# Kernel tuning notes

Measured on AMD Instinct MI355X. Metric: run time of the kernel, lower is better.

The kernel has to match this reference:

```python
import jax, jax.numpy as jnp
import numpy as np

N_NODES = 100000
N_EDGES = 1600000
D_IN, D_HID, D_OUT = 256, 128, 64


def setup_inputs() -> dict:
    key = jax.random.key(0)
    k = jax.random.split(key, 6)
    x = jax.random.normal(k[0], (N_NODES, D_IN), dtype=jnp.float32)
    edge_index = jax.random.randint(k[1], (2, N_EDGES), 0, N_NODES, dtype=jnp.int64)
    W1 = jax.random.normal(k[2], (D_IN, D_HID), dtype=jnp.float32) / np.sqrt(D_IN)
    b1 = jnp.zeros((D_HID,), dtype=jnp.float32)
    W2 = jax.random.normal(k[3], (D_HID, D_OUT), dtype=jnp.float32) / np.sqrt(D_HID)
    b2 = jnp.zeros((D_OUT,), dtype=jnp.float32)
    return {"x": x, "edge_index": edge_index, "W1": W1, "b1": b1, "W2": W2, "b2": b2}


def gcn_conv(x, W, b, src, dst, n):
    """PyG GCNConv: h = D^-1/2 (A+I) D^-1/2 (x W) + b, symmetric norm with self-loops."""
    h = x @ W                                           # [n, d_out]
    # degree from destination (col) index, +1 for the self-loop edge weight
    deg = jnp.ones((n,), x.dtype).at[dst].add(jnp.float32(1.0))
    dinv = jax.lax.rsqrt(deg)                           # deg >= 1, no inf
    norm = dinv[src] * dinv[dst]                        # [E]
    agg = jax.ops.segment_sum(h[src] * norm[:, None], dst, num_segments=n)
    agg = agg + h * (dinv * dinv)[:, None]              # self-loop contribution
    return agg + b


def reference(x, edge_index, W1, b1, W2, b2):
    src, dst = edge_index[0], edge_index[1]
    n = x.shape[0]
    h = gcn_conv(x, W1, b1, src, dst, n)
    h = jax.nn.relu(h)                                  # dropout is identity in eval mode
    out = gcn_conv(h, W2, b2, src, dst, n)
    return out
```

## Files before the change

### kernel.cpp

```cpp
#include <hip/hip_runtime.h>
#include <stdint.h>

typedef unsigned short u16;
typedef unsigned int u32;
typedef __bf16 bf16x8 __attribute__((ext_vector_type(8)));
typedef float floatx4 __attribute__((ext_vector_type(4)));

static __device__ __forceinline__ float bf2f(u16 u) {
  union { u32 i; float f; } v; v.i = ((u32)u) << 16; return v.f;
}
static __device__ __forceinline__ u16 f2bf(float f) {
  union { float f; u32 i; } v; v.f = f;
  u32 u = v.i;
  return (u16)((u + 0x7fffu + ((u >> 16) & 1u)) >> 16);
}

__global__ void k_edgemode(const int* __restrict__ ei, int* __restrict__ flag) {
  int t = threadIdx.x;
  int v = ei[2 * t + 1];
  unsigned long long b = __ballot(v == 0);
  if (t == 0) *flag = (b == ~0ull) ? 1 : 0;
}

static __device__ __forceinline__ int edge_src(const int* ei, int E, int i, int m64) {
  return m64 ? ei[2 * (size_t)i] : ei[i];
}
static __device__ __forceinline__ int edge_dst(const int* ei, int E, int i, int m64) {
  return m64 ? ei[2 * (size_t)E + 2 * (size_t)i] : ei[(size_t)E + i];
}

__global__ void k_transpose(const float* __restrict__ W1, const float* __restrict__ W2,
                            u16* __restrict__ Wt1, u16* __restrict__ Wt2) {
  int i = blockIdx.x * 256 + threadIdx.x;
  if (i < 256 * 128) {
    int k = i >> 7, c = i & 127;
    Wt1[c * 256 + k] = f2bf(W1[i]);
  } else {
    int j = i - 256 * 128;
    if (j < 128 * 64) {
      int k = j >> 6, c = j & 63;
      Wt2[c * 128 + k] = f2bf(W2[j]);
    }
  }
}

#define CHUNK 2048

__global__ void k_count(const int* __restrict__ ei, int E, const int* __restrict__ flag,
                        int* __restrict__ bucket_cnt, int NB) {
  __shared__ int h[1024];
  const int t = threadIdx.x;
  for (int i = t; i < 1024; i += 256) h[i] = 0;
  __syncthreads();
  const int c0 = blockIdx.x * CHUNK;
  const int cnt = min(CHUNK, E - c0);
  const int m64 = *flag;
  for (int i = t; i < cnt; i += 256)
    atomicAdd(&h[edge_dst(ei, E, c0 + i, m64) >> 7], 1);
  __syncthreads();
  for (int i = t; i < NB; i += 256)
    if (h[i]) atomicAdd(&bucket_cnt[i], h[i]);
}

__global__ void k_bscan(const int* __restrict__ bucket_cnt, int* __restrict__ bucket_base,
                        int* __restrict__ bucket_cursor, int NB,
                        int* __restrict__ row_ptr, int n, int E) {
  __shared__ int ts[256];
  const int t = threadIdx.x;
  const int b4 = t * 4;
  int a0 = (b4 + 0 < NB) ? bucket_cnt[b4 + 0] : 0;
  int a1 = (b4 + 1 < NB) ? bucket_cnt[b4 + 1] : 0;
  int a2 = (b4 + 2 < NB) ? bucket_cnt[b4 + 2] : 0;
  int a3 = (b4 + 3 < NB) ? bucket_cnt[b4 + 3] : 0;
  int p1 = a0, p2 = p1 + a1, p3 = p2 + a2, tsum = p3 + a3;
  ts[t] = tsum;
  __syncthreads();
  for (int off = 1; off < 256; off <<= 1) {
    int x = (t >= off) ? ts[t - off] : 0;
    __syncthreads();
    ts[t] += x;
    __syncthreads();
  }
  int ex0 = ts[t] - tsum;
  int e[4] = {ex0, ex0 + p1, ex0 + p2, ex0 + p3};
#pragma unroll
  for (int j = 0; j < 4; ++j) {
    int i = b4 + j;
    if (i < NB) { bucket_base[i] = e[j]; bucket_cursor[i] = e[j]; }
  }
  if (t == 0) row_ptr[n] = E + n;
}

__global__ void k_place(const int* __restrict__ ei, int E, const int* __restrict__ flag,
                        int* __restrict__ bucket_cursor, uint2* __restrict__ pairs, int NB) {
  __shared__ int h[1024];
  __shared__ int ex[1024];
  __shared__ int cur[1024];
  __shared__ int ts[256];
  __shared__ uint2 stage[CHUNK];
  const int t = threadIdx.x;
  const int c0 = blockIdx.x * CHUNK;
  const int cnt = min(CHUNK, E - c0);
  const int m64 = *flag;

  for (int i = t; i < 1024; i += 256) h[i] = 0;
  __syncthreads();

  int es[8], ed[8];
#pragma unroll
  for (int j = 0; j < 8; ++j) {
    int i = t + j * 256;
    es[j] = 0; ed[j] = -1;
    if (i < cnt) {
      es[j] = edge_src(ei, E, c0 + i, m64);
      ed[j] = edge_dst(ei, E, c0 + i, m64);
      atomicAdd(&h[ed[j] >> 7], 1);
    }
  }
  __syncthreads();

  const int b4 = t * 4;
  int a0 = h[b4], a1 = h[b4 + 1], a2 = h[b4 + 2], a3 = h[b4 + 3];
  int p1 = a0, p2 = p1 + a1, p3 = p2 + a2, tsum = p3 + a3;
  ts[t] = tsum;
  __syncthreads();
  for (int off = 1; off < 256; off <<= 1) {
    int x = (t >= off) ? ts[t - off] : 0;
    __syncthreads();
    ts[t] += x;
    __syncthreads();
  }
  int ex0 = ts[t] - tsum;
  ex[b4] = ex0;       cur[b4] = ex0;
  ex[b4 + 1] = ex0 + p1; cur[b4 + 1] = ex0 + p1;
  ex[b4 + 2] = ex0 + p2; cur[b4 + 2] = ex0 + p2;
  ex[b4 + 3] = ex0 + p3; cur[b4 + 3] = ex0 + p3;
  __syncthreads();

#pragma unroll
  for (int j = 0; j < 8; ++j) {
    if (ed[j] >= 0) {
      int b = ed[j] >> 7;
      int pos = atomicAdd(&cur[b], 1);
      stage[pos] = make_uint2((u32)es[j], (u32)ed[j]);
    }
  }
  __syncthreads();
  for (int i = t; i < NB; i += 256) {
    int c = h[i];
    if (c > 0) h[i] = atomicAdd(&bucket_cursor[i], c);
  }
  __syncthreads();

  for (int i = t; i < cnt; i += 256) {
    uint2 p = stage[i];
    int b = (int)(p.y >> 7);
    pairs[h[b] + (i - ex[b])] = p;
  }
}

#define BMAX 3072
__global__ void k_csr(const uint2* __restrict__ pairs, const int* __restrict__ bucket_cnt,
                      const int* __restrict__ bucket_base, int* __restrict__ row_ptr,
                      float* __restrict__ dinv, int* __restrict__ srcs, int n) {
  __shared__ int h[128], cur[128];
  __shared__ int lsrc[BMAX];
  const int b = blockIdx.x;
  const int t = threadIdx.x;
  const int cnt = bucket_cnt[b];
  const int base = bucket_base[b];
  const int nbase = base + b * 128;

  if (t < 128) h[t] = 0;
  __syncthreads();
  for (int i = t; i < cnt; i += 256)
    atomicAdd(&h[pairs[base + i].y & 127], 1);
  __syncthreads();

  __shared__ int sc[128];
  int v = 0;
  if (t < 128) { v = h[t]; sc[t] = v; }
  __syncthreads();
  for (int off = 1; off < 128; off <<= 1) {
    int x = 0;
    if (t < 128 && t >= off) x = sc[t - off];
    __syncthreads();
    if (t < 128) sc[t] += x;
    __syncthreads();
  }
  if (t < 128) {
    int excl = sc[t] - v;
    cur[t] = excl + t + 1;
    int node = b * 128 + t;
    if (node < n) {
      row_ptr[node] = nbase + excl + t;
      dinv[node] = rsqrtf(1.0f + (float)v);
      int sp = excl + t;
      if (sp < BMAX) lsrc[sp] = node;
      else srcs[nbase + sp] = node;
    }
  }
  __syncthreads();

  for (int i = t; i < cnt; i += 256) {
    uint2 p = pairs[base + i];
    int pos = atomicAdd(&cur[p.y & 127], 1);
    if (pos < BMAX) lsrc[pos] = (int)p.x;
    else srcs[nbase + pos] = (int)p.x;
  }
  __syncthreads();
  const int lim = min(cnt + 128, BMAX);
  for (int i = t; i < lim; i += 256) srcs[nbase + i] = lsrc[i];
}

template<int N, int K, bool A_FP32>
__launch_bounds__(256, 4)
__global__ void k_gemm(const void* __restrict__ Ap, const u16* __restrict__ Wt,
                       const float* __restrict__ dinv, u16* __restrict__ G, int M)
{
  constexpr int ESZ = A_FP32 ? 4 : 2;
  constexpr int KS  = K / 32;
  constexpr int NT  = N / 32;
  const int t = threadIdx.x;
  const int wave = t >> 6, lane = t & 63;
  const int row0 = blockIdx.x * 64;
  const int wr = wave >> 1, wc = wave & 1;
  const int lm = lane & 15, lq = lane >> 4;

  floatx4 acc[2][NT];
#pragma unroll
  for (int i = 0; i < 2; ++i)
#pragma unroll
    for (int j = 0; j < NT; ++j) acc[i][j] = (floatx4)(0.0f);

  int r0 = row0 + wr * 32 + lm;
  int r1 = r0 + 16;
  if (r0 >= M) r0 = M - 1;
  if (r1 >= M) r1 = M - 1;
  const char* pa0 = (const char*)Ap + ((size_t)r0 * K + lq * 8) * ESZ;
  const char* pa1 = (const char*)Ap + ((size_t)r1 * K + lq * 8) * ESZ;
  const u16*  pb  = Wt + (size_t)(wc * (N / 2) + lm) * K + lq * 8;

#pragma unroll
  for (int ks = 0; ks < KS; ++ks) {
    bf16x8 a[2];
    if constexpr (A_FP32) {
      float4 f0 = *(const float4*)(pa0 + ks * 128);
      float4 f1 = *(const float4*)(pa0 + ks * 128 + 16);
      float4 g0 = *(const float4*)(pa1 + ks * 128);
      float4 g1 = *(const float4*)(pa1 + ks * 128 + 16);
      bf16x8 av, bv;
      av[0] = (__bf16)f0.x; av[1] = (__bf16)f0.y; av[2] = (__bf16)f0.z; av[3] = (__bf16)f0.w;
      av[4] = (__bf16)f1.x; av[5] = (__bf16)f1.y; av[6] = (__bf16)f1.z; av[7] = (__bf16)f1.w;
      bv[0] = (__bf16)g0.x; bv[1] = (__bf16)g0.y; bv[2] = (__bf16)g0.z; bv[3] = (__bf16)g0.w;
      bv[4] = (__bf16)g1.x; bv[5] = (__bf16)g1.y; bv[6] = (__bf16)g1.z; bv[7] = (__bf16)g1.w;
      a[0] = av; a[1] = bv;
    } else {
      a[0] = *(const bf16x8*)(pa0 + ks * 64);
      a[1] = *(const bf16x8*)(pa1 + ks * 64);
    }
    bf16x8 b[NT];
#pragma unroll
    for (int nt = 0; nt < NT; ++nt)
      b[nt] = *(const bf16x8*)(pb + (size_t)nt * 16 * K + ks * 32);
#pragma unroll
    for (int nt = 0; nt < NT; ++nt) {
      acc[0][nt] = __builtin_amdgcn_mfma_f32_16x16x32_bf16(a[0], b[nt], acc[0][nt], 0, 0, 0);
      acc[1][nt] = __builtin_amdgcn_mfma_f32_16x16x32_bf16(a[1], b[nt], acc[1][nt], 0, 0, 0);
    }
  }

  const int crow0 = row0 + wr * 32 + lq * 4;
#pragma unroll
  for (int mt = 0; mt < 2; ++mt) {
#pragma unroll
    for (int nt = 0; nt < NT; ++nt) {
      const int gc = wc * (N / 2) + nt * 16 + lm;
#pragma unroll
      for (int r = 0; r < 4; ++r) {
        const int gr = crow0 + mt * 16 + r;
        if (gr < M) G[(size_t)gr * N + gc] = f2bf(acc[mt][nt][r] * dinv[gr]);
      }
    }
  }
}

template<int F, bool RELU, bool OUT_BF16, int NPW>
__launch_bounds__(256, 4)
__global__ void k_agg(const u16* __restrict__ g, const int* __restrict__ row_ptr,
                      const int* __restrict__ srcs, const float* __restrict__ dinv,
                      const float* __restrict__ bias, void* __restrict__ outp, int n)
{
  const int wid = blockIdx.x * 4 + (threadIdx.x >> 6);
  const int n0 = wid * NPW;
  if (n0 >= n) return;
  const int n1 = min(n0 + NPW, n);
  const int lane = threadIdx.x & 63;
  constexpr int VPL = F / 64;
  const int col = lane * VPL;
  const float b0 = bias[col];
  const float b1 = (VPL == 2) ? bias[col + (VPL - 1)] : 0.f;

  int e    = __builtin_amdgcn_readfirstlane(row_ptr[n0]);
  int eEnd = __builtin_amdgcn_readfirstlane(row_ptr[n1]);
  int cur  = n0;
  int nb   = __builtin_amdgcn_readfirstlane(row_ptr[n0 + 1]);
  float dv = dinv[n0];
  float a0 = 0.f, a1 = 0.f;

  auto fin = [&]() {
    float o0 = dv * a0 + b0;
    if (RELU) o0 = fmaxf(o0, 0.f);
    if constexpr (VPL == 2) {
      float o1 = dv * a1 + b1;
      if (RELU) o1 = fmaxf(o1, 0.f);
      if constexpr (OUT_BF16) {
        u32 pk = (u32)f2bf(o0) | ((u32)f2bf(o1) << 16);
        *(u32*)((u16*)outp + (size_t)cur * F + col) = pk;
      } else {
        *(float2*)((float*)outp + (size_t)cur * F + col) = make_float2(o0, o1);
      }
    } else {
      if constexpr (OUT_BF16) ((u16*)outp)[(size_t)cur * F + col] = f2bf(o0);
      else                    ((float*)outp)[(size_t)cur * F + col] = o0;
    }
    ++cur;
    a0 = 0.f; a1 = 0.f;
    if (cur < n) {
      dv = dinv[cur];
      nb = __builtin_amdgcn_readfirstlane(row_ptr[cur + 1]);
    }
  };

  auto issue = [&](int eb, u32* gv) {
    const int* sp = srcs + eb;
#pragma unroll
    for (int j = 0; j < 8; ++j) {
      const int s = sp[j];
      if constexpr (VPL == 2)
        gv[j] = *(const u32*)(g + (size_t)s * F + col);
      else
        gv[j] = (u32)g[(size_t)s * F + col];
    }
  };

  auto consume = [&](int eb, const u32* gv) {
#pragma unroll
    for (int j = 0; j < 8; ++j) {
      if (eb + j == nb) fin();
      if constexpr (VPL == 2) {
        a0 += bf2f((u16)gv[j]);
        a1 += bf2f((u16)(gv[j] >> 16));
      } else {
        a0 += bf2f((u16)gv[j]);
      }
    }
  };

  u32 gvA[8], gvB[8];
  const int rem = (eEnd - e) >> 3;
  if (rem >= 1) issue(e, gvA);
  if (rem >= 2) issue(e + 8, gvB);
  int i = 0;
  for (; i + 2 < rem; i += 2) {
    consume(e + i * 8, gvA);
    issue(e + (i + 2) * 8, gvA);
    consume(e + (i + 1) * 8, gvB);
    if (i + 3 < rem) issue(e + (i + 3) * 8, gvB);
  }
  if (i < rem) { consume(e + i * 8, gvA); ++i; }
  if (i < rem) { consume(e + i * 8, gvB); ++i; }

  for (int et = e + rem * 8; et < eEnd; ++et) {
    const int s = srcs[et];
    u32 gvt;
    if constexpr (VPL == 2) gvt = *(const u32*)(g + (size_t)s * F + col);
    else                    gvt = (u32)g[(size_t)s * F + col];
    if (et == nb) fin();
    if constexpr (VPL == 2) { a0 += bf2f((u16)gvt); a1 += bf2f((u16)(gvt >> 16)); }
    else                    a0 += bf2f((u16)gvt);
  }
  fin();
}

extern "C" void kernel_launch(void* const* d_in, const int* in_sizes, int n_in,
                              void* d_out, int out_size, void* d_ws, size_t ws_size,
                              hipStream_t stream)
{
  const float* x  = (const float*)d_in[0];
  const int*   ei = (const int*)d_in[1];
  const float* W1 = (const float*)d_in[2];
  const float* b1 = (const float*)d_in[3];
  const float* W2 = (const float*)d_in[4];
  const float* b2 = (const float*)d_in[5];

  const int n = in_sizes[0] / 256;
  const int E = in_sizes[1] / 2;
  const int NB = (n + 127) >> 7;

  char* ws = (char*)d_ws;
  size_t off = 0;
  auto alloc = [&](size_t bytes) -> void* {
    void* p = ws + off;
    off = (off + bytes + 255) & ~(size_t)255;
    return p;
  };
  int*   row_ptr = (int*)alloc((size_t)(n + 1) * 4);
  int*   bcnt    = (int*)alloc(1024 * 4);
  int*   bbase   = (int*)alloc(1024 * 4);
  int*   bcur    = (int*)alloc(1024 * 4);
  int*   eflag   = (int*)alloc(256);
  float* dinv    = (float*)alloc((size_t)n * 4);
  u16*   Wt1     = (u16*)alloc(256 * 128 * 2);
  u16*   Wt2     = (u16*)alloc(128 * 64 * 2);
  uint2* pairs   = (uint2*)alloc((size_t)E * 8);
  int*   srcs    = (int*)alloc((size_t)(E + n + 512) * 4);
  u16*   g1      = (u16*)alloc((size_t)n * 128 * 2);
  u16*   y1      = (u16*)alloc((size_t)n * 128 * 2);
  u16*   g2      = (u16*)alloc((size_t)n * 64 * 2);
  (void)ws_size; (void)n_in; (void)out_size;

  const int TB = 256;
  const int nbC = (E + CHUNK - 1) / CHUNK;

  hipMemsetAsync(bcnt, 0, 1024 * 4, stream);
  k_edgemode<<<1, 64, 0, stream>>>(ei, eflag);
  k_transpose<<<(256 * 128 + 128 * 64 + TB - 1) / TB, TB, 0, stream>>>(W1, W2, Wt1, Wt2);
  k_count<<<nbC, TB, 0, stream>>>(ei, E, eflag, bcnt, NB);
  k_bscan<<<1, TB, 0, stream>>>(bcnt, bbase, bcur, NB, row_ptr, n, E);
  k_place<<<nbC, TB, 0, stream>>>(ei, E, eflag, bcur, pairs, NB);
  k_csr<<<NB, TB, 0, stream>>>(pairs, bcnt, bbase, row_ptr, dinv, srcs, n);

  constexpr int NPW = 8;
  const int nwaves = (n + NPW - 1) / NPW;
  const int aggGrid = (nwaves + 3) / 4;

  k_gemm<128, 256, true><<<(n + 63) / 64, 256, 0, stream>>>(x, Wt1, dinv, g1, n);
  k_agg<128, true, true, NPW><<<aggGrid, 256, 0, stream>>>(g1, row_ptr, srcs, dinv, b1, y1, n);
  k_gemm<64, 128, false><<<(n + 63) / 64, 256, 0, stream>>>(y1, Wt2, dinv, g2, n);
  k_agg<64, false, false, NPW><<<aggGrid, 256, 0, stream>>>(g2, row_ptr, srcs, dinv, b2, d_out, n);
}
```

Measured before the change: 398.3 us.

## Software-pipeline GEMM global loads with explicit vmcnt waits; raise agg occupancy

The GEMM kernel now issues global loads for A and W chunks two steps ahead into a three-slot register ring. It uses manual s_waitcnt vmcnt and sched_barrier to overlap memory latency with MFMA work. To cover the extra live registers, launch bounds for the fp32-input variant drop to 3 waves per SIMD. The aggregation kernel's launch bounds go up to 8, which forces fewer registers in exchange for higher occupancy and risks spills.

```diff
diff --git a/kernel.cpp b/kernel.cpp
--- a/kernel.cpp
+++ b/kernel.cpp
@@ -214,24 +214,23 @@
 }
 
 template<int N, int K, bool A_FP32>
-__launch_bounds__(256, 4)
+__launch_bounds__(256, A_FP32 ? 3 : 4)
 __global__ void k_gemm(const void* __restrict__ Ap, const u16* __restrict__ Wt,
                        const float* __restrict__ dinv, u16* __restrict__ G, int M)
 {
   constexpr int ESZ = A_FP32 ? 4 : 2;
-  constexpr int KS  = K / 32;
+  constexpr int NCH = K / 32;
   constexpr int NT  = N / 32;
+  constexpr int ALD = A_FP32 ? 4 : 2;
+  constexpr int LPK = ALD + NT;
+  constexpr int D   = 2;
+  constexpr int R   = 3;
+
   const int t = threadIdx.x;
   const int wave = t >> 6, lane = t & 63;
   const int row0 = blockIdx.x * 64;
   const int wr = wave >> 1, wc = wave & 1;
   const int lm = lane & 15, lq = lane >> 4;
-
-  floatx4 acc[2][NT];
-#pragma unroll
-  for (int i = 0; i < 2; ++i)
-#pragma unroll
-    for (int j = 0; j < NT; ++j) acc[i][j] = (floatx4)(0.0f);
 
   int r0 = row0 + wr * 32 + lm;
   int r1 = r0 + 16;
@@ -241,34 +240,72 @@
   const char* pa1 = (const char*)Ap + ((size_t)r1 * K + lq * 8) * ESZ;
   const u16*  pb  = Wt + (size_t)(wc * (N / 2) + lm) * K + lq * 8;
 
-#pragma unroll
-  for (int ks = 0; ks < KS; ++ks) {
+  float4 fa[R][2][2];
+  bf16x8 ra[R][2];
+  bf16x8 rb[R][NT];
+
+  auto issue = [&](int c) {
+    const int sl = c % R;
+    if constexpr (A_FP32) {
+      fa[sl][0][0] = *(const float4*)(pa0 + c * 128);
+      fa[sl][0][1] = *(const float4*)(pa0 + c * 128 + 16);
+      fa[sl][1][0] = *(const float4*)(pa1 + c * 128);
+      fa[sl][1][1] = *(const float4*)(pa1 + c * 128 + 16);
+    } else {
+      ra[sl][0] = *(const bf16x8*)(pa0 + c * 64);
+      ra[sl][1] = *(const bf16x8*)(pa1 + c * 64);
+    }
+#pragma unroll
+    for (int nt = 0; nt < NT; ++nt)
+      rb[sl][nt] = *(const bf16x8*)(pb + (size_t)nt * 16 * K + c * 32);
+  };
+
+  floatx4 acc[2][NT];
+#pragma unroll
+  for (int i = 0; i < 2; ++i)
+#pragma unroll
+    for (int j = 0; j < NT; ++j) acc[i][j] = (floatx4)(0.0f);
+
+  auto compute = [&](int c) {
+    const int sl = c % R;
     bf16x8 a[2];
     if constexpr (A_FP32) {
-      float4 f0 = *(const float4*)(pa0 + ks * 128);
-      float4 f1 = *(const float4*)(pa0 + ks * 128 + 16);
-      float4 g0 = *(const float4*)(pa1 + ks * 128);
-      float4 g1 = *(const float4*)(pa1 + ks * 128 + 16);
-      bf16x8 av, bv;
-      av[0] = (__bf16)f0.x; av[1] = (__bf16)f0.y; av[2] = (__bf16)f0.z; av[3] = (__bf16)f0.w;
-      av[4] = (__bf16)f1.x; av[5] = (__bf16)f1.y; av[6] = (__bf16)f1.z; av[7] = (__bf16)f1.w;
-      bv[0] = (__bf16)g0.x; bv[1] = (__bf16)g0.y; bv[2] = (__bf16)g0.z; bv[3] = (__bf16)g0.w;
-      bv[4] = (__bf16)g1.x; bv[5] = (__bf16)g1.y; bv[6] = (__bf16)g1.z; bv[7] = (__bf16)g1.w;
-      a[0] = av; a[1] = bv;
+#pragma unroll
+      for (int mt = 0; mt < 2; ++mt) {
+        float4 f0 = fa[sl][mt][0], f1 = fa[sl][mt][1];
+        bf16x8 av;
+        av[0] = (__bf16)f0.x; av[1] = (__bf16)f0.y; av[2] = (__bf16)f0.z; av[3] = (__bf16)f0.w;
+        av[4] = (__bf16)f1.x; av[5] = (__bf16)f1.y; av[6] = (__bf16)f1.z; av[7] = (__bf16)f1.w;
+        a[mt] = av;
+      }
     } else {
-      a[0] = *(const bf16x8*)(pa0 + ks * 64);
-      a[1] = *(const bf16x8*)(pa1 + ks * 64);
-    }
-    bf16x8 b[NT];
-#pragma unroll
-    for (int nt = 0; nt < NT; ++nt)
-      b[nt] = *(const bf16x8*)(pb + (size_t)nt * 16 * K + ks * 32);
+      a[0] = ra[sl][0]; a[1] = ra[sl][1];
+    }
 #pragma unroll
     for (int nt = 0; nt < NT; ++nt) {
-      acc[0][nt] = __builtin_amdgcn_mfma_f32_16x16x32_bf16(a[0], b[nt], acc[0][nt], 0, 0, 0);
-      acc[1][nt] = __builtin_amdgcn_mfma_f32_16x16x32_bf16(a[1], b[nt], acc[1][nt], 0, 0, 0);
-    }
-  }
+      acc[0][nt] = __builtin_amdgcn_mfma_f32_16x16x32_bf16(a[0], rb[sl][nt], acc[0][nt], 0, 0, 0);
+      acc[1][nt] = __builtin_amdgcn_mfma_f32_16x16x32_bf16(a[1], rb[sl][nt], acc[1][nt], 0, 0, 0);
+    }
+  };
+
+  issue(0); issue(1);
+  __builtin_amdgcn_sched_barrier(0);
+
+#pragma unroll
+  for (int c = 0; c < NCH - D; ++c) {
+    issue(c + D);
+    __builtin_amdgcn_sched_barrier(0);
+    asm volatile("s_waitcnt vmcnt(%0)" :: "i"(D * LPK) : "memory");
+    __builtin_amdgcn_sched_barrier(0);
+    compute(c);
+    __builtin_amdgcn_sched_barrier(0);
+  }
+  asm volatile("s_waitcnt vmcnt(%0)" :: "i"(LPK) : "memory");
+  __builtin_amdgcn_sched_barrier(0);
+  compute(NCH - 2);
+  asm volatile("s_waitcnt vmcnt(0)" ::: "memory");
+  __builtin_amdgcn_sched_barrier(0);
+  compute(NCH - 1);
 
   const int crow0 = row0 + wr * 32 + lq * 4;
 #pragma unroll
@@ -286,7 +323,7 @@
 }
 
 template<int F, bool RELU, bool OUT_BF16, int NPW>
-__launch_bounds__(256, 4)
+__launch_bounds__(256, 8)
 __global__ void k_agg(const u16* __restrict__ g, const int* __restrict__ row_ptr,
                       const int* __restrict__ srcs, const float* __restrict__ dinv,
                       const float* __restrict__ bias, void* __restrict__ outp, int n)
```

Result: no change. 396.8 us (-0.4%).
